# Performance work log

Measured on AMD Instinct MI355X. Metric: run time of the kernel, lower is better.

The kernel has to match this reference:

```python
import jax, jax.numpy as jnp
import numpy as np

NUM_VECTORS = 8192
LATENT_DIM = 256
BETA = 0.25


def setup_inputs() -> dict:
    key = jax.random.key(0)
    k1, k2 = jax.random.split(key)
    z = jax.random.normal(k1, (16, LATENT_DIM, 32, 32), dtype=jnp.float32)
    # nn.Embedding weight initialized uniform(-1/K, 1/K)
    emb_weight = jax.random.uniform(
        k2, (NUM_VECTORS, LATENT_DIM), dtype=jnp.float32,
        minval=-1.0 / NUM_VECTORS, maxval=1.0 / NUM_VECTORS)
    return {"z": z, "emb_weight": emb_weight}


def reference(z, emb_weight):
    # z: [B, C, H, W] -> [B, H, W, C]
    z_bhwc = jnp.transpose(z, (0, 2, 3, 1))
    B, H, W, C = z_bhwc.shape
    z_flat = z_bhwc.reshape(-1, C)  # [N, C]

    # Squared distances: ||z||^2 + ||e||^2 - 2 z.e  -> [N, K]
    d = (jnp.sum(z_flat ** 2, axis=1, keepdims=True)
         + jnp.sum(emb_weight ** 2, axis=1)
         - 2.0 * jnp.einsum('nc,kc->nk', z_flat, emb_weight))
    idx = jnp.argmin(d, axis=1)  # [N]

    z_q = emb_weight[idx].reshape(B, H, W, C)

    sg = jax.lax.stop_gradient
    loss = (jnp.mean((sg(z_q) - z_bhwc) ** 2)
            + BETA * jnp.mean((z_q - sg(z_bhwc)) ** 2))

    # Straight-through estimator
    z_q_st = z_bhwc + sg(z_q - z_bhwc)
    z_q_out = jnp.transpose(z_q_st, (0, 3, 1, 2))  # [B, C, H, W]
    return z_q_out, idx, loss
```

## Files before the change

kernel.cpp:

```cpp
#include <hip/hip_runtime.h>
#include <math.h>

#define NB   16
#define CC   256
#define NPTS 16384
#define KK   8192
#define Z_OUT 4194304

#define WS_ENORM 16448
#define WS_CCNT  24640
#define WS_CIDX  41024
#define CAND_CAP 64
#define LCAP     96
#define MARGIN   4.0e-4f

typedef short v8s __attribute__((ext_vector_type(8)));
typedef float v4f __attribute__((ext_vector_type(4)));

__device__ __forceinline__ void gl_lds16(const void* g, void* l) {
    __builtin_amdgcn_global_load_lds((const __attribute__((address_space(1))) void*)g,
                                     (__attribute__((address_space(3))) void*)l, 16, 0, 0);
}
__device__ __forceinline__ unsigned short f2bf(float f) {
    unsigned int u = __float_as_uint(f);
    return (unsigned short)((u + 0x7FFFu + ((u >> 16) & 1u)) >> 16);
}
__device__ __forceinline__ unsigned fenc(float f) {
    unsigned u = __float_as_uint(f);
    return (u & 0x80000000u) ? ~u : (u | 0x80000000u);
}
__device__ __forceinline__ float fdec(unsigned m) {
    unsigned u = (m & 0x80000000u) ? (m & 0x7fffffffu) : ~m;
    return __uint_as_float(u);
}

__global__ void k_prep(const float* __restrict__ z, const float* __restrict__ emb,
                       unsigned short* __restrict__ zb16, unsigned short* __restrict__ ebf,
                       float* __restrict__ enorm, float* __restrict__ lossAcc,
                       int* __restrict__ doneCnt) {
    const int bid = blockIdx.x;
    const int tid = threadIdx.x;
    if (bid < 2048) {
        const int w = tid >> 6, lane = tid & 63;
        const int k = bid * 4 + w;
        const int i = k * CC + lane * 4;
        float4 v = *(const float4*)(emb + i);
        *(ushort4*)(ebf + i) = make_ushort4(f2bf(v.x), f2bf(v.y), f2bf(v.z), f2bf(v.w));
        float s = v.x * v.x + v.y * v.y + v.z * v.z + v.w * v.w;
        for (int off = 32; off > 0; off >>= 1) s += __shfl_down(s, off);
        if (lane == 0) enorm[k] = s;
        if (bid == 0 && tid == 0) { lossAcc[0] = 0.0f; doneCnt[0] = 0; }
    } else {
        __shared__ float ts[64][65];
        const int b2 = bid - 2048;
        const int hw0 = (b2 & 15) * 64, c0 = ((b2 >> 4) & 3) * 64, b = b2 >> 6;
#pragma unroll
        for (int p = 0; p < 4; ++p) {
            int u = p * 256 + tid;
            int ci = u >> 4, j4 = (u & 15) << 2;
            float4 v = *(const float4*)(z + (size_t)b * 262144 + (size_t)(c0 + ci) * 1024 + hw0 + j4);
            ts[ci][j4 + 0] = v.x; ts[ci][j4 + 1] = v.y; ts[ci][j4 + 2] = v.z; ts[ci][j4 + 3] = v.w;
        }
        __syncthreads();
#pragma unroll
        for (int p = 0; p < 4; ++p) {
            int u = p * 256 + tid;
            int hj = u >> 4, i4 = (u & 15) << 2;
            ushort4 o = make_ushort4(f2bf(ts[i4 + 0][hj]), f2bf(ts[i4 + 1][hj]),
                                     f2bf(ts[i4 + 2][hj]), f2bf(ts[i4 + 3][hj]));
            *(ushort4*)(zb16 + (size_t)(b * 1024 + hw0 + hj) * 256 + c0 + i4) = o;
        }
    }
}

__global__ __launch_bounds__(512, 2)
void k_cand(const unsigned short* __restrict__ zb16, const unsigned short* __restrict__ ebf,
            int* __restrict__ candCnt, int* __restrict__ candI) {
    __shared__ short    Bs[8][4][512];
    __shared__ unsigned runmaxU[64];
    __shared__ int      cnt[64];
    __shared__ int      lstK[64][LCAP];
    __shared__ float    lstD[64][LCAP];

    const int tid  = threadIdx.x;
    const int lane = tid & 63;
    const int w    = tid >> 6;
    const int nb   = blockIdx.x << 6;
    const int m16  = lane & 15, q = lane >> 4;

    if (tid < 64) { runmaxU[tid] = 0x007FFFFFu;  cnt[tid] = 0; }

#pragma unroll
    for (int p = 0; p < 4; ++p) {
        const int g8 = p * 8 + w;
        const int cc = g8 >> 2, nt = g8 & 3;
        const unsigned short* g = zb16 + (size_t)(nb + nt * 16 + m16) * 256 + cc * 32 + q * 8;
        gl_lds16(g, &Bs[cc][nt][lane * 8]);
    }

    auto loadA = [&](v8s (&a)[4], int kbr, int cc) {
#pragma unroll
        for (int kt = 0; kt < 4; ++kt)
            a[kt] = *(const v8s*)(ebf + (size_t)(kbr + (kt << 4) + m16) * 256 + (cc << 5) + q * 8);
    };
    auto loadB = [&](v8s (&b)[4], int cc) {
#pragma unroll
        for (int nt = 0; nt < 4; ++nt) b[nt] = *(const v8s*)&Bs[cc][nt][lane * 8];
    };

    v8s aR[4][4];
    v8s bP[4], bN[4];

    const int kb0 = w << 6;
    loadA(aR[0], kb0, 0);
    loadA(aR[1], kb0, 1);
    loadA(aR[2], kb0, 2);
    __syncthreads();
    loadB(bP, 0);

#pragma unroll 1
    for (int s = 0; s < 16; ++s) {
        const int kb  = ((s << 3) + w) << 6;
        const int kbn = (s < 15) ? kb + 512 : kb;
        v4f acc[16];
#pragma unroll
        for (int i = 0; i < 16; ++i) acc[i] = (v4f){0.f, 0.f, 0.f, 0.f};

#pragma unroll
        for (int cc = 0; cc < 8; ++cc) {
            if ((cc & 1) == 0) loadB(bN, (cc + 1) & 7);
            else               loadB(bP, (cc + 1) & 7);
            {
                const int tcc = cc + 3;
                if (tcc < 8) loadA(aR[tcc & 3], kb,  tcc);
                else         loadA(aR[tcc & 3], kbn, tcc - 8);
            }
#pragma unroll
            for (int kt = 0; kt < 4; ++kt)
#pragma unroll
                for (int nt = 0; nt < 4; ++nt)
                    acc[kt * 4 + nt] = __builtin_amdgcn_mfma_f32_16x16x32_bf16(
                        aR[cc & 3][kt], ((cc & 1) ? bN[nt] : bP[nt]),
                        acc[kt * 4 + nt], 0, 0, 0);
        }

        float mx[4];
#pragma unroll
        for (int nt = 0; nt < 4; ++nt) {
            float m = acc[0 * 4 + nt][0];
#pragma unroll
            for (int kt = 0; kt < 4; ++kt)
#pragma unroll
                for (int r = 0; r < 4; ++r) m = fmaxf(m, acc[kt * 4 + nt][r]);
            m = fmaxf(m, __shfl_xor(m, 16));
            m = fmaxf(m, __shfl_xor(m, 32));
            mx[nt] = m;
            if (lane < 16) atomicMax(&runmaxU[nt * 16 + lane], fenc(m));
        }
#pragma unroll
        for (int nt = 0; nt < 4; ++nt) {
            const int nl = nt * 16 + m16;
            const float thr = fmaxf(fdec(runmaxU[nl]), mx[nt]) - MARGIN;
#pragma unroll
            for (int kt = 0; kt < 4; ++kt)
#pragma unroll
                for (int r = 0; r < 4; ++r) {
                    if (acc[kt * 4 + nt][r] >= thr) {
                        int k = kb + (kt << 4) + q * 4 + r;
                        int pos = atomicAdd(&cnt[nl], 1);
                        if (pos < LCAP) { lstK[nl][pos] = k; lstD[nl][pos] = acc[kt * 4 + nt][r]; }
                    }
                }
        }
        if (s == 3 || s == 9) __syncthreads();
    }

    __syncthreads();
    if (tid < 64) {
        const int n = nb + tid;
        const int c = cnt[tid];
        if (c > LCAP) {
            candCnt[n] = KK;
        } else {
            const float thr = fdec(runmaxU[tid]) - MARGIN;
            int kept = 0;
            for (int i = 0; i < c; ++i) {
                if (lstD[tid][i] >= thr) {
                    if (kept < CAND_CAP) candI[(size_t)n * CAND_CAP + kept] = lstK[tid][i];
                    ++kept;
                }
            }
            candCnt[n] = (kept > CAND_CAP) ? KK : kept;
        }
    }
}

__global__ __launch_bounds__(256)
void k_final(const float* __restrict__ z, const float* __restrict__ emb,
             const float* __restrict__ enorm, const int* __restrict__ candCnt,
             const int* __restrict__ candI, float* __restrict__ out,
             float* __restrict__ idxf, float* __restrict__ lossAcc,
             int* __restrict__ doneCnt, float* __restrict__ outLoss) {
    __shared__ float zl[16][261];
    __shared__ int   kis[16];
    __shared__ float red[256];
    const int bid = blockIdx.x;
    const int b = bid >> 6, hw0 = (bid & 63) << 4;
    const int tid = threadIdx.x;
    const int lane = tid & 63, w = tid >> 6;

#pragma unroll
    for (int p = 0; p < 4; ++p) {
        const int u = p * 256 + tid;
        const int c = u >> 2, j4 = (u & 3) << 2;
        float4 v = *(const float4*)(z + (size_t)b * 262144 + (size_t)c * 1024 + hw0 + j4);
        zl[j4 + 0][c] = v.x; zl[j4 + 1][c] = v.y; zl[j4 + 2][c] = v.z; zl[j4 + 3][c] = v.w;
    }
    __syncthreads();

#pragma unroll 1
    for (int rr = 0; rr < 4; ++rr) {
        const int j = w * 4 + rr;
        const int n = b * 1024 + hw0 + j;
        const float4 zv = *(const float4*)&zl[j][lane * 4];
        float zn = zv.x * zv.x;
        zn = fmaf(zv.y, zv.y, zn); zn = fmaf(zv.z, zv.z, zn); zn = fmaf(zv.w, zv.w, zn);
#pragma unroll
        for (int off = 1; off < 64; off <<= 1) zn += __shfl_xor(zn, off);
        const int cnt = candCnt[n];
        float bd = __builtin_inff();
        int   bk = 0x7fffffff;
        if (cnt <= CAND_CAP) {
            int myk = 0;
            if (lane < cnt) myk = candI[(size_t)n * CAND_CAP + lane];
            if (cnt > 0) {
                int kc = __shfl(myk, 0);
                float4 ev = *(const float4*)(emb + (size_t)kc * CC + lane * 4);
#pragma unroll 1
                for (int i = 0; i < cnt; ++i) {
                    const float4 evc = ev;
                    const int kcur = kc;
                    if (i + 1 < cnt) {
                        kc = __shfl(myk, i + 1);
                        ev = *(const float4*)(emb + (size_t)kc * CC + lane * 4);
                    }
                    float p = zv.x * evc.x;
                    p = fmaf(zv.y, evc.y, p);
                    p = fmaf(zv.z, evc.z, p);
                    p = fmaf(zv.w, evc.w, p);
#pragma unroll
                    for (int off = 1; off < 64; off <<= 1) p += __shfl_xor(p, off);
                    const float d = (zn + enorm[kcur]) - (p + p);
                    if (d < bd || (d == bd && kcur < bk)) { bd = d; bk = kcur; }
                }
            }
        } else {
#pragma unroll 1
            for (int k = 0; k < KK; ++k) {
                const float4 ev = *(const float4*)(emb + (size_t)k * CC + lane * 4);
                float p = zv.x * ev.x;
                p = fmaf(zv.y, ev.y, p);
                p = fmaf(zv.z, ev.z, p);
                p = fmaf(zv.w, ev.w, p);
#pragma unroll
                for (int off = 1; off < 64; off <<= 1) p += __shfl_xor(p, off);
                const float d = (zn + enorm[k]) - (p + p);
                if (d < bd) { bd = d; bk = k; }
            }
        }
        if (lane == 0) { idxf[n] = (float)bk; kis[j] = bk; }
    }
    __syncthreads();

    const int j  = tid & 15;
    const int cg = tid >> 4;
    const int ki0 = kis[j];
    const float* ep = emb + (size_t)ki0 * CC;
    float ls = 0.0f;
#pragma unroll 4
    for (int c = cg * 16; c < cg * 16 + 16; ++c) {
        float e  = ep[c];
        float zv = zl[j][c];
        out[(size_t)b * 262144 + (size_t)c * 1024 + hw0 + j] = e;
        float df = e - zv;
        ls = fmaf(df, df, ls);
    }
    red[tid] = ls;
    __syncthreads();
    for (int s2 = 128; s2 > 0; s2 >>= 1) {
        if (tid < s2) red[tid] += red[tid + s2];
        __syncthreads();
    }
    if (tid == 0) {
        atomicAdd(lossAcc, red[0]);
        __threadfence();
        int old = atomicAdd(doneCnt, 1);
        if (old == (int)gridDim.x - 1) {
            float tot = atomicAdd(lossAcc, 0.0f);
            float m = tot * (1.0f / 4194304.0f);
            outLoss[0] = m + 0.25f * m;
        }
    }
}

extern "C" void kernel_launch(void* const* d_in, const int* in_sizes, int n_in,
                              void* d_out, int out_size, void* d_ws, size_t ws_size,
                              hipStream_t stream) {
    const float* z   = (const float*)d_in[0];
    const float* emb = (const float*)d_in[1];
    float* outf = (float*)d_out;
    float* wsf  = (float*)d_ws;

    float* lossAcc = wsf;
    int*   doneCnt = (int*)(wsf + 1);
    float* enorm   = wsf + WS_ENORM;
    int*   candCnt = (int*)(wsf + WS_CCNT);
    int*   candI   = (int*)(wsf + WS_CIDX);

    unsigned short* zb16 = (unsigned short*)outf;
    unsigned short* ebf  = (unsigned short*)(outf + 2097152);

    k_prep<<<3072, 256, 0, stream>>>(z, emb, zb16, ebf, enorm, lossAcc, doneCnt);
    k_cand<<<256, 512, 0, stream>>>(zb16, ebf, candCnt, candI);
    k_final<<<1024, 256, 0, stream>>>(z, emb, enorm, candCnt, candI,
                                      outf, outf + Z_OUT, lossAcc, doneCnt,
                                      outf + Z_OUT + NPTS);
}
```

Measured before the change: 268.5 us.

## Fuse candidate rescoring into k_cand and split out a lightweight gather kernel

Result: faster. 255.3 us (-4.9%).

```diff
diff --git a/kernel.cpp b/kernel.cpp
--- a/kernel.cpp
+++ b/kernel.cpp
@@ -8,9 +8,6 @@
 #define Z_OUT 4194304
 
 #define WS_ENORM 16448
-#define WS_CCNT  24640
-#define WS_CIDX  41024
-#define CAND_CAP 64
 #define LCAP     96
 #define MARGIN   4.0e-4f
 
@@ -75,12 +72,14 @@
 
 __global__ __launch_bounds__(512, 2)
 void k_cand(const unsigned short* __restrict__ zb16, const unsigned short* __restrict__ ebf,
-            int* __restrict__ candCnt, int* __restrict__ candI) {
+            const float* __restrict__ z, const float* __restrict__ emb,
+            const float* __restrict__ enorm, float* __restrict__ idxf) {
     __shared__ short    Bs[8][4][512];
     __shared__ unsigned runmaxU[64];
     __shared__ int      cnt[64];
     __shared__ int      lstK[64][LCAP];
     __shared__ float    lstD[64][LCAP];
+    __shared__ float    zl[64][257];
 
     const int tid  = threadIdx.x;
     const int lane = tid & 63;
@@ -176,83 +175,62 @@
     }
 
     __syncthreads();
-    if (tid < 64) {
-        const int n = nb + tid;
-        const int c = cnt[tid];
-        if (c > LCAP) {
-            candCnt[n] = KK;
-        } else {
-            const float thr = fdec(runmaxU[tid]) - MARGIN;
-            int kept = 0;
-            for (int i = 0; i < c; ++i) {
-                if (lstD[tid][i] >= thr) {
-                    if (kept < CAND_CAP) candI[(size_t)n * CAND_CAP + kept] = lstK[tid][i];
-                    ++kept;
-                }
-            }
-            candCnt[n] = (kept > CAND_CAP) ? KK : kept;
-        }
-    }
-}
-
-__global__ __launch_bounds__(256)
-void k_final(const float* __restrict__ z, const float* __restrict__ emb,
-             const float* __restrict__ enorm, const int* __restrict__ candCnt,
-             const int* __restrict__ candI, float* __restrict__ out,
-             float* __restrict__ idxf, float* __restrict__ lossAcc,
-             int* __restrict__ doneCnt, float* __restrict__ outLoss) {
-    __shared__ float zl[16][261];
-    __shared__ int   kis[16];
-    __shared__ float red[256];
-    const int bid = blockIdx.x;
-    const int b = bid >> 6, hw0 = (bid & 63) << 4;
-    const int tid = threadIdx.x;
-    const int lane = tid & 63, w = tid >> 6;
-
-#pragma unroll
-    for (int p = 0; p < 4; ++p) {
-        const int u = p * 256 + tid;
-        const int c = u >> 2, j4 = (u & 3) << 2;
-        float4 v = *(const float4*)(z + (size_t)b * 262144 + (size_t)c * 1024 + hw0 + j4);
-        zl[j4 + 0][c] = v.x; zl[j4 + 1][c] = v.y; zl[j4 + 2][c] = v.z; zl[j4 + 3][c] = v.w;
+
+    {
+        const int b = nb >> 10, hw0 = nb & 1023;
+#pragma unroll
+        for (int p = 0; p < 8; ++p) {
+            const int u = p * 512 + tid;
+            const int c = u >> 4, j4 = (u & 15) << 2;
+            float4 v = *(const float4*)(z + (size_t)b * 262144 + (size_t)c * 1024 + hw0 + j4);
+            zl[j4 + 0][c] = v.x; zl[j4 + 1][c] = v.y; zl[j4 + 2][c] = v.z; zl[j4 + 3][c] = v.w;
+        }
     }
     __syncthreads();
 
 #pragma unroll 1
-    for (int rr = 0; rr < 4; ++rr) {
-        const int j = w * 4 + rr;
-        const int n = b * 1024 + hw0 + j;
-        const float4 zv = *(const float4*)&zl[j][lane * 4];
+    for (int rr = 0; rr < 8; ++rr) {
+        const int nl = w * 8 + rr;
+        const int n  = nb + nl;
+        const float4 zv = *(const float4*)&zl[nl][lane * 4];
         float zn = zv.x * zv.x;
         zn = fmaf(zv.y, zv.y, zn); zn = fmaf(zv.z, zv.z, zn); zn = fmaf(zv.w, zv.w, zn);
 #pragma unroll
         for (int off = 1; off < 64; off <<= 1) zn += __shfl_xor(zn, off);
-        const int cnt = candCnt[n];
+        const int cl = cnt[nl];
         float bd = __builtin_inff();
         int   bk = 0x7fffffff;
-        if (cnt <= CAND_CAP) {
-            int myk = 0;
-            if (lane < cnt) myk = candI[(size_t)n * CAND_CAP + lane];
-            if (cnt > 0) {
-                int kc = __shfl(myk, 0);
-                float4 ev = *(const float4*)(emb + (size_t)kc * CC + lane * 4);
-#pragma unroll 1
-                for (int i = 0; i < cnt; ++i) {
-                    const float4 evc = ev;
-                    const int kcur = kc;
-                    if (i + 1 < cnt) {
-                        kc = __shfl(myk, i + 1);
-                        ev = *(const float4*)(emb + (size_t)kc * CC + lane * 4);
-                    }
-                    float p = zv.x * evc.x;
-                    p = fmaf(zv.y, evc.y, p);
-                    p = fmaf(zv.z, evc.z, p);
-                    p = fmaf(zv.w, evc.w, p);
-#pragma unroll
-                    for (int off = 1; off < 64; off <<= 1) p += __shfl_xor(p, off);
-                    const float d = (zn + enorm[kcur]) - (p + p);
-                    if (d < bd || (d == bd && kcur < bk)) { bd = d; bk = kcur; }
-                }
+        if (cl <= 64) {
+            int  ki = 0;
+            bool pass = false;
+            if (lane < cl) {
+                ki = lstK[nl][lane];
+                pass = (lstD[nl][lane] >= fdec(runmaxU[nl]) - MARGIN);
+            }
+            unsigned long long mask = __ballot(pass);
+            int kc = -1;
+            float4 ev;
+            if (mask) {
+                const int j0 = __ffsll(mask) - 1; mask &= mask - 1;
+                kc = __shfl(ki, j0);
+                ev = *(const float4*)(emb + (size_t)kc * CC + lane * 4);
+            }
+            while (kc >= 0) {
+                const int    kcur = kc;
+                const float4 evc  = ev;
+                if (mask) {
+                    const int jn = __ffsll(mask) - 1; mask &= mask - 1;
+                    kc = __shfl(ki, jn);
+                    ev = *(const float4*)(emb + (size_t)kc * CC + lane * 4);
+                } else kc = -1;
+                float p = zv.x * evc.x;
+                p = fmaf(zv.y, evc.y, p);
+                p = fmaf(zv.z, evc.z, p);
+                p = fmaf(zv.w, evc.w, p);
+#pragma unroll
+                for (int off = 1; off < 64; off <<= 1) p += __shfl_xor(p, off);
+                const float d = (zn + enorm[kcur]) - (p + p);
+                if (d < bd || (d == bd && kcur < bk)) { bd = d; bk = kcur; }
             }
         } else {
 #pragma unroll 1
@@ -268,30 +246,41 @@
                 if (d < bd) { bd = d; bk = k; }
             }
         }
-        if (lane == 0) { idxf[n] = (float)bk; kis[j] = bk; }
-    }
-    __syncthreads();
-
-    const int j  = tid & 15;
-    const int cg = tid >> 4;
-    const int ki0 = kis[j];
-    const float* ep = emb + (size_t)ki0 * CC;
+        if (lane == 0) idxf[n] = (float)bk;
+    }
+}
+
+__global__ __launch_bounds__(256)
+void k_gather(const float* __restrict__ z, const float* __restrict__ emb,
+              const float* __restrict__ idxf, float* __restrict__ out,
+              float* __restrict__ lossAcc, int* __restrict__ doneCnt,
+              float* __restrict__ outLoss) {
+    __shared__ float red[256];
+    const int bid = blockIdx.x;
+    const int b = bid >> 5, h = bid & 31;
+    const int t = threadIdx.x;
+    const int w_ = t & 31, cg = t >> 5;
+    const int n = b * 1024 + h * 32 + w_;
+    const int ki = (int)idxf[n];
+    const float* ep = emb + (size_t)ki * CC;
+    const size_t base = (size_t)b * 262144 + h * 32 + w_;
     float ls = 0.0f;
 #pragma unroll 4
-    for (int c = cg * 16; c < cg * 16 + 16; ++c) {
-        float e  = ep[c];
-        float zv = zl[j][c];
-        out[(size_t)b * 262144 + (size_t)c * 1024 + hw0 + j] = e;
+    for (int c = cg; c < CC; c += 8) {
+        float e = ep[c];
+        size_t a = base + (size_t)c * 1024;
+        float zv = z[a];
+        out[a] = e;
         float df = e - zv;
         ls = fmaf(df, df, ls);
     }
-    red[tid] = ls;
+    red[t] = ls;
     __syncthreads();
-    for (int s2 = 128; s2 > 0; s2 >>= 1) {
-        if (tid < s2) red[tid] += red[tid + s2];
+    for (int s = 128; s > 0; s >>= 1) {
+        if (t < s) red[t] += red[t + s];
         __syncthreads();
     }
-    if (tid == 0) {
+    if (t == 0) {
         atomicAdd(lossAcc, red[0]);
         __threadfence();
         int old = atomicAdd(doneCnt, 1);
@@ -314,15 +303,12 @@
     float* lossAcc = wsf;
     int*   doneCnt = (int*)(wsf + 1);
     float* enorm   = wsf + WS_ENORM;
-    int*   candCnt = (int*)(wsf + WS_CCNT);
-    int*   candI   = (int*)(wsf + WS_CIDX);
 
     unsigned short* zb16 = (unsigned short*)outf;
     unsigned short* ebf  = (unsigned short*)(outf + 2097152);
 
     k_prep<<<3072, 256, 0, stream>>>(z, emb, zb16, ebf, enorm, lossAcc, doneCnt);
-    k_cand<<<256, 512, 0, stream>>>(zb16, ebf, candCnt, candI);
-    k_final<<<1024, 256, 0, stream>>>(z, emb, enorm, candCnt, candI,
-                                      outf, outf + Z_OUT, lossAcc, doneCnt,
-                                      outf + Z_OUT + NPTS);
-}
+    k_cand<<<256, 512, 0, stream>>>(zb16, ebf, z, emb, enorm, outf + Z_OUT);
+    k_gather<<<512, 256, 0, stream>>>(z, emb, outf + Z_OUT, outf,
+                                      lossAcc, doneCnt, outf + Z_OUT + NPTS);
+}
```
